# Performance work log

Measured on AMD Instinct MI355X. Metric: run time of the kernel, lower is better.

Reference implementation:

```python
import jax, jax.numpy as jnp
import numpy as np

RADIUS = 0.1
NSAMPLE = 32


def ball_query_cnt(radius, nsample, xyz, new_xyz):
    """xyz: (B,N,3), new_xyz: (B,npoint,3) -> cnt (B,npoint) int32, idx (B,npoint,nsample) int32.
    Matches pointnet2 CUDA semantics: first `nsample` in-radius points in index order;
    unfilled slots replicate the first found index (0 if none found)."""
    N = xyz.shape[1]
    # (B, npoint, N) squared distances
    d2 = jnp.sum((new_xyz[:, :, None, :] - xyz[:, None, :, :]) ** 2, axis=-1)
    mask = d2 < radius * radius
    pos = jnp.arange(N, dtype=jnp.int32)
    # key encodes position so that top_k returns the LOWEST valid positions first
    key = jnp.where(mask, N - pos, -N)
    topk_vals, _ = jax.lax.top_k(key, nsample)          # (B, npoint, nsample)
    valid = topk_vals > 0
    idx = (N - topk_vals).astype(jnp.int32)
    first = jnp.where(valid[..., :1], idx[..., :1], 0)   # fill value per query
    idx = jnp.where(valid, idx, first)
    cnt = jnp.minimum(mask.sum(axis=-1), nsample).astype(jnp.int32)
    return cnt, idx


def group(features, idx):
    """features: (B,C,N), idx: (B,npoint,nsample) -> (B,C,npoint,nsample)."""
    return jax.vmap(lambda f, i: f[:, i])(features, idx)


def setup_inputs() -> dict:
    key = jax.random.key(0)
    k1, k2, k3 = jax.random.split(key, 3)
    B, N, npoint, C = 4, 16384, 2048, 64
    xyz = jax.random.uniform(k1, (B, N, 3), dtype=jnp.float32)
    new_xyz = jax.random.uniform(k2, (B, npoint, 3), dtype=jnp.float32)
    features = jax.random.normal(k3, (B, C, N), dtype=jnp.float32)
    return {"xyz": xyz, "new_xyz": new_xyz, "features": features}


def reference(xyz, new_xyz, features):
    idx_cnt, idx = ball_query_cnt(RADIUS, NSAMPLE, xyz, new_xyz)
    xyz_t = jnp.transpose(xyz, (0, 2, 1))                      # (B,3,N)
    grouped_xyz = group(xyz_t, idx)                            # (B,3,npoint,nsample)
    grouped_xyz = grouped_xyz - jnp.transpose(new_xyz, (0, 2, 1))[..., None]
    grouped_features = group(features, idx)                    # (B,C,npoint,nsample)
    new_features = jnp.concatenate([grouped_xyz, grouped_features], axis=1)
    return idx_cnt, new_features
```

## Files before the change

kernel.cpp:

```cpp
#include <hip/hip_runtime.h>

#define B        4
#define N        16384
#define NPOINT   2048
#define C        64
#define NSAMPLE  32
#define CH       (C + 3)
#define RADIUS2  0.01f
#define NCELL    1000
#define CSTRIDE  1032
#define CCSTRIDE 1024
#define CAP      192

__device__ __forceinline__ int clamp10(int v) {
    return v < 0 ? 0 : (v > 9 ? 9 : v);
}

__global__ __launch_bounds__(256) void transpose_count_kernel(
    const float* __restrict__ xyz,
    const float* __restrict__ f,
    float* __restrict__ ft,
    int* __restrict__ cc)
{
    const int t = threadIdx.x;

    if (blockIdx.x >= 1024) {
        const int g = (blockIdx.x - 1024) * 256 + t;
        const int b = g >> 14;
        const float x = xyz[g * 3 + 0], y = xyz[g * 3 + 1], z = xyz[g * 3 + 2];
        const int cx = clamp10((int)(x * 10.f));
        const int cy = clamp10((int)(y * 10.f));
        const int cz = clamp10((int)(z * 10.f));
        atomicAdd(&cc[(b << 10) + (cx * 10 + cy) * 10 + cz], 1);
        return;
    }

    const int tt = blockIdx.x;
    const int b  = tt >> 8;
    const int n0 = (tt & 255) * 64;

    __shared__ float tile[64][65];
    const int r16 = t >> 4;
    const int x4  = t & 15;
    #pragma unroll
    for (int it = 0; it < 4; ++it) {
        const int cch = it * 16 + r16;
        const float4 v = *(const float4*)(f + ((size_t)b * C + cch) * N + n0 + x4 * 4);
        tile[cch][x4 * 4 + 0] = v.x;
        tile[cch][x4 * 4 + 1] = v.y;
        tile[cch][x4 * 4 + 2] = v.z;
        tile[cch][x4 * 4 + 3] = v.w;
    }
    __syncthreads();
    #pragma unroll
    for (int it = 0; it < 4; ++it) {
        const int nn = it * 16 + r16;
        float4 v;
        v.x = tile[x4 * 4 + 0][nn];
        v.y = tile[x4 * 4 + 1][nn];
        v.z = tile[x4 * 4 + 2][nn];
        v.w = tile[x4 * 4 + 3][nn];
        *(float4*)(ft + ((size_t)b * N + n0 + nn) * C + x4 * 4) = v;
    }
}

__global__ __launch_bounds__(1024) void prefix_kernel(int* __restrict__ cnt,
                                                      int* __restrict__ cs) {
    __shared__ int s[1024];
    const int t = threadIdx.x, b = blockIdx.x;
    const int v = (t < NCELL) ? cnt[(b << 10) + t] : 0;
    s[t] = v;
    __syncthreads();
    for (int off = 1; off < 1024; off <<= 1) {
        const int u = (t >= off) ? s[t - off] : 0;
        __syncthreads();
        s[t] += u;
        __syncthreads();
    }
    const int excl = (t == 0) ? 0 : s[t - 1];
    if (t <= NCELL) cs[b * CSTRIDE + t] = excl;
    if (t < NCELL)  cnt[(b << 10) + t] = excl;
}

__global__ __launch_bounds__(256) void scatter_kernel(const float* __restrict__ xyz,
                                                      int* __restrict__ cursor,
                                                      float4* __restrict__ sp) {
    const int g = blockIdx.x * 256 + threadIdx.x;
    const int b = g >> 14;
    const int n = g & (N - 1);
    const float x = xyz[g * 3 + 0], y = xyz[g * 3 + 1], z = xyz[g * 3 + 2];
    const int cx = clamp10((int)(x * 10.f));
    const int cy = clamp10((int)(y * 10.f));
    const int cz = clamp10((int)(z * 10.f));
    const int cell = (cx * 10 + cy) * 10 + cz;
    const int pos = atomicAdd(&cursor[(b << 10) + cell], 1);
    sp[(b << 14) + pos] = make_float4(x, y, z, __int_as_float(n));
}

__global__ __launch_bounds__(256, 8) void qg_kernel(
    const float*  __restrict__ xyz,
    const float*  __restrict__ new_xyz,
    const float*  __restrict__ ft,
    const int*    __restrict__ cs,
    const float4* __restrict__ sp,
    float* __restrict__ out_cnt,
    float* __restrict__ out_feat)
{
    const int w = threadIdx.x >> 6;
    const int l = threadIdx.x & 63;
    const int q = blockIdx.x * 4 + w;
    const int b = q >> 11;
    const int j = q & (NPOINT - 1);

    __shared__ int cand_s[4][CAP];
    __shared__ int sidx_s[4][NSAMPLE];
    int* cand  = cand_s[w];
    int* s_idx = sidx_s[w];

    const float qx = new_xyz[q * 3 + 0];
    const float qy = new_xyz[q * 3 + 1];
    const float qz = new_xyz[q * 3 + 2];

    const int cx = clamp10((int)(qx * 10.f));
    const int cy = clamp10((int)(qy * 10.f));
    const int cz = clamp10((int)(qz * 10.f));
    const int z0 = cz > 0 ? cz - 1 : 0;
    const int z1 = cz < 9 ? cz + 1 : 9;

    int sv = 0, ev = 0;
    if (l < 9) {
        const int xx = cx - 1 + l / 3;
        const int yy = cy - 1 + l % 3;
        if (xx >= 0 && xx <= 9 && yy >= 0 && yy <= 9) {
            const int cb = (xx * 10 + yy) * 10;
            sv = cs[b * CSTRIDE + cb + z0];
            ev = cs[b * CSTRIDE + cb + z1 + 1];
        }
    }
    const int len = ev - sv;

    int S[9], L[9];
    #pragma unroll
    for (int r = 0; r < 9; ++r) {
        S[r] = __builtin_amdgcn_readlane(sv, r);
        L[r] = __builtin_amdgcn_readlane(len, r);
    }
    int T = 0;
    #pragma unroll
    for (int r = 0; r < 9; ++r) T += L[r];

    const unsigned long long ltmask = (1ull << l) - 1ull;
    int total = 0, ncand = 0;
    for (int base = 0; base < T; base += 64) {
        const int wid = base + l;
        int p = 0, acc = 0;
        bool act = false;
        #pragma unroll
        for (int r = 0; r < 9; ++r) {
            const int off = wid - acc;
            if (off >= 0 && off < L[r]) { p = S[r] + off; act = true; }
            acc += L[r];
        }
        float4 pt = make_float4(1e9f, 1e9f, 1e9f, 0.f);
        if (act) pt = sp[(b << 14) + p];
        const float dx = pt.x - qx, dy = pt.y - qy, dz = pt.z - qz;
        const float d2 = dx * dx + dy * dy + dz * dz;
        const bool in = act && (d2 < RADIUS2);
        const unsigned long long m = __ballot(in);
        if (in) {
            const int slot = ncand + __popcll(m & ltmask);
            if (slot < CAP) cand[slot] = __float_as_int(pt.w);
        }
        const int c = __popcll(m);
        total += c;
        ncand = ncand + c > CAP ? CAP : ncand + c;
    }

    int cntv;
    if (total > CAP) {
        const float* xb = xyz + (size_t)b * N * 3;
        int cnt2 = 0;
        for (int base = 0; base < N; base += 64) {
            const int p = base + l;
            const float dx = xb[p * 3 + 0] - qx;
            const float dy = xb[p * 3 + 1] - qy;
            const float dz = xb[p * 3 + 2] - qz;
            const float d2 = dx * dx + dy * dy + dz * dz;
            const bool in = d2 < RADIUS2;
            const unsigned long long m = __ballot(in);
            if (in) {
                const int slot = cnt2 + __popcll(m & ltmask);
                if (slot < NSAMPLE) s_idx[slot] = p;
            }
            cnt2 += __popcll(m);
            if (cnt2 >= NSAMPLE) break;
        }
        cntv = cnt2 < NSAMPLE ? cnt2 : NSAMPLE;
        __threadfence_block();
    } else {
        __threadfence_block();
        const int K = ncand;
        for (int c = l; c < K; c += 64) {
            const int v = cand[c];
            int rnk = 0;
            for (int i = 0; i < K; ++i) rnk += (cand[i] < v) ? 1 : 0;
            if (rnk < NSAMPLE) s_idx[rnk] = v;
        }
        cntv = total < NSAMPLE ? total : NSAMPLE;
        __threadfence_block();
    }

    if (l < NSAMPLE && l >= cntv) s_idx[l] = (cntv > 0) ? s_idx[0] : 0;
    __threadfence_block();

    if (l == 0) out_cnt[q] = (float)cntv;

    const int k   = l & 31;
    const int i   = s_idx[k];
    const int chh = l >> 5;

    if (l < 32) {
        const float* xp = xyz + ((size_t)b * N + i) * 3;
        float* ob = out_feat + ((size_t)(b * CH) * NPOINT + j) * NSAMPLE + l;
        __builtin_nontemporal_store(xp[0] - qx, ob);
        __builtin_nontemporal_store(xp[1] - qy, ob + NPOINT * NSAMPLE);
        __builtin_nontemporal_store(xp[2] - qz, ob + 2 * NPOINT * NSAMPLE);
    }
    const float* fp = ft + ((size_t)b * N + i) * C + chh;
    float* op = out_feat + ((size_t)(b * CH + 3 + chh) * NPOINT + j) * NSAMPLE + k;
    #pragma unroll 8
    for (int p = 0; p < 32; ++p) {
        __builtin_nontemporal_store(fp[2 * p],
                                    op + (size_t)2 * p * NPOINT * NSAMPLE);
    }
}

__global__ __launch_bounds__(64) void qg_wave_kernel(
    const float* __restrict__ xyz,
    const float* __restrict__ new_xyz,
    const float* __restrict__ feat,
    float* __restrict__ out_cnt,
    float* __restrict__ out_feat)
{
    const int q = blockIdx.x;
    const int b = q >> 11;
    const int j = q & (NPOINT - 1);
    const int l = threadIdx.x;

    __shared__ int s_idx[NSAMPLE];

    const float qx = new_xyz[q * 3 + 0];
    const float qy = new_xyz[q * 3 + 1];
    const float qz = new_xyz[q * 3 + 2];
    const float* xb = xyz + (size_t)b * N * 3;

    int cnt = 0;
    for (int base = 0; base < N; base += 64) {
        const int p = base + l;
        const float dx = xb[p * 3 + 0] - qx;
        const float dy = xb[p * 3 + 1] - qy;
        const float dz = xb[p * 3 + 2] - qz;
        const float d2 = dx * dx + dy * dy + dz * dz;
        const bool in = d2 < RADIUS2;
        const unsigned long long m = __ballot(in);
        if (in) {
            const int slot = cnt + __popcll(m & ((1ull << l) - 1ull));
            if (slot < NSAMPLE) s_idx[slot] = p;
        }
        cnt += __popcll(m);
        if (cnt >= NSAMPLE) break;
    }
    if (cnt > NSAMPLE) cnt = NSAMPLE;

    if (l == 0) out_cnt[q] = (float)cnt;
    __syncthreads();
    if (l < NSAMPLE && l >= cnt) s_idx[l] = (cnt > 0) ? s_idx[0] : 0;
    __syncthreads();

    const int k   = l & 31;
    const int i   = s_idx[k];
    const int chh = l >> 5;
    if (l < 32) {
        const float* xp = xyz + ((size_t)b * N + i) * 3;
        float* ob = out_feat + ((size_t)(b * CH) * NPOINT + j) * NSAMPLE + l;
        ob[0]                   = xp[0] - qx;
        ob[NPOINT * NSAMPLE]     = xp[1] - qy;
        ob[2 * NPOINT * NSAMPLE] = xp[2] - qz;
    }
    const float* fp = feat + ((size_t)b * C + chh) * N + i;
    float* op = out_feat + ((size_t)(b * CH + 3 + chh) * NPOINT + j) * NSAMPLE + k;
    #pragma unroll 8
    for (int p = 0; p < 32; ++p) {
        op[(size_t)2 * p * NPOINT * NSAMPLE] = fp[(size_t)2 * p * N];
    }
}

extern "C" void kernel_launch(void* const* d_in, const int* in_sizes, int n_in,
                              void* d_out, int out_size, void* d_ws, size_t ws_size,
                              hipStream_t stream) {
    const float* xyz      = (const float*)d_in[0];
    const float* new_xyz  = (const float*)d_in[1];
    const float* features = (const float*)d_in[2];

    float* out_cnt  = (float*)d_out;
    float* out_feat = out_cnt + (size_t)B * NPOINT;

    char* ws = (char*)d_ws;
    const size_t ftB = (size_t)B * N * C * sizeof(float);
    const size_t spB = (size_t)B * N * sizeof(float4);
    const size_t csB = (size_t)B * CSTRIDE * sizeof(int);
    const size_t ccB = (size_t)B * CCSTRIDE * sizeof(int);
    const size_t need = ftB + spB + csB + ccB;

    if (ws_size >= need) {
        float*  ft = (float*)ws;
        float4* sp = (float4*)(ws + ftB);
        int*    cs = (int*)(ws + ftB + spB);
        int*    cc = (int*)(ws + ftB + spB + csB);
        hipMemsetAsync(cc, 0, ccB, stream);
        transpose_count_kernel<<<1280, 256, 0, stream>>>(xyz, features, ft, cc);
        prefix_kernel<<<B, 1024, 0, stream>>>(cc, cs);
        scatter_kernel<<<B * N / 256, 256, 0, stream>>>(xyz, cc, sp);
        qg_kernel<<<B * NPOINT / 4, 256, 0, stream>>>(xyz, new_xyz, ft, cs, sp,
                                                      out_cnt, out_feat);
    } else {
        qg_wave_kernel<<<B * NPOINT, 64, 0, stream>>>(xyz, new_xyz, features,
                                                      out_cnt, out_feat);
    }
}
```

Before: 137.7 us.

## Fuse prefix scan into prep kernel via last-block pattern; vectorize gather stores

Merges the transpose/count kernel and the per-batch prefix-scan kernel into one launch. A last-block-done atomic counter (stored in the unused cc[1023] slot) elects one block to run the scan over all four batches. The gather epilogue now has each lane produce a float4 of four consecutive samples for one channel and write it with a single 16-byte nontemporal store, where before each lane wrote scalars. This saves one kernel launch and widens the output writes, at the cost of a serialized single-block scan and a device-wide fence in every block.

Result: slower. 247.7 us (+79.9%).

```diff
diff --git a/kernel.cpp b/kernel.cpp
--- a/kernel.cpp
+++ b/kernel.cpp
@@ -11,18 +11,25 @@
 #define CSTRIDE  1032
 #define CCSTRIDE 1024
 #define CAP      192
+#define K1GRID   1280
+
+typedef float vfloat4 __attribute__((ext_vector_type(4)));
 
 __device__ __forceinline__ int clamp10(int v) {
     return v < 0 ? 0 : (v > 9 ? 9 : v);
 }
 
-__global__ __launch_bounds__(256) void transpose_count_kernel(
+__global__ __launch_bounds__(256) void prep_kernel(
     const float* __restrict__ xyz,
     const float* __restrict__ f,
     float* __restrict__ ft,
-    int* __restrict__ cc)
+    int* __restrict__ cc,
+    int* __restrict__ cs)
 {
     const int t = threadIdx.x;
+    __shared__ float tile[64][65];
+    __shared__ int   wsum[256];
+    __shared__ int   islast;
 
     if (blockIdx.x >= 1024) {
         const int g = (blockIdx.x - 1024) * 256 + t;
@@ -32,54 +39,74 @@
         const int cy = clamp10((int)(y * 10.f));
         const int cz = clamp10((int)(z * 10.f));
         atomicAdd(&cc[(b << 10) + (cx * 10 + cy) * 10 + cz], 1);
-        return;
-    }
-
-    const int tt = blockIdx.x;
-    const int b  = tt >> 8;
-    const int n0 = (tt & 255) * 64;
-
-    __shared__ float tile[64][65];
-    const int r16 = t >> 4;
-    const int x4  = t & 15;
-    #pragma unroll
-    for (int it = 0; it < 4; ++it) {
-        const int cch = it * 16 + r16;
-        const float4 v = *(const float4*)(f + ((size_t)b * C + cch) * N + n0 + x4 * 4);
-        tile[cch][x4 * 4 + 0] = v.x;
-        tile[cch][x4 * 4 + 1] = v.y;
-        tile[cch][x4 * 4 + 2] = v.z;
-        tile[cch][x4 * 4 + 3] = v.w;
-    }
+    } else {
+        const int tt = blockIdx.x;
+        const int b  = tt >> 8;
+        const int n0 = (tt & 255) * 64;
+        const int r16 = t >> 4;
+        const int x4  = t & 15;
+        #pragma unroll
+        for (int it = 0; it < 4; ++it) {
+            const int cch = it * 16 + r16;
+            const float4 v = *(const float4*)(f + ((size_t)b * C + cch) * N + n0 + x4 * 4);
+            tile[cch][x4 * 4 + 0] = v.x;
+            tile[cch][x4 * 4 + 1] = v.y;
+            tile[cch][x4 * 4 + 2] = v.z;
+            tile[cch][x4 * 4 + 3] = v.w;
+        }
+        __syncthreads();
+        #pragma unroll
+        for (int it = 0; it < 4; ++it) {
+            const int nn = it * 16 + r16;
+            float4 v;
+            v.x = tile[x4 * 4 + 0][nn];
+            v.y = tile[x4 * 4 + 1][nn];
+            v.z = tile[x4 * 4 + 2][nn];
+            v.w = tile[x4 * 4 + 3][nn];
+            *(float4*)(ft + ((size_t)b * N + n0 + nn) * C + x4 * 4) = v;
+        }
+    }
+
+    __threadfence();
     __syncthreads();
-    #pragma unroll
-    for (int it = 0; it < 4; ++it) {
-        const int nn = it * 16 + r16;
-        float4 v;
-        v.x = tile[x4 * 4 + 0][nn];
-        v.y = tile[x4 * 4 + 1][nn];
-        v.z = tile[x4 * 4 + 2][nn];
-        v.w = tile[x4 * 4 + 3][nn];
-        *(float4*)(ft + ((size_t)b * N + n0 + nn) * C + x4 * 4) = v;
-    }
-}
-
-__global__ __launch_bounds__(1024) void prefix_kernel(int* __restrict__ cnt,
-                                                      int* __restrict__ cs) {
-    __shared__ int s[1024];
-    const int t = threadIdx.x, b = blockIdx.x;
-    const int v = (t < NCELL) ? cnt[(b << 10) + t] : 0;
-    s[t] = v;
+    if (t == 0) {
+        const int done = atomicAdd(&cc[1023], 1);
+        islast = (done == K1GRID - 1) ? 1 : 0;
+    }
     __syncthreads();
-    for (int off = 1; off < 1024; off <<= 1) {
-        const int u = (t >= off) ? s[t - off] : 0;
+    if (!islast) return;
+
+    for (int bb = 0; bb < B; ++bb) {
+        int h[4];
+        #pragma unroll
+        for (int m = 0; m < 4; ++m) {
+            const int cell = t * 4 + m;
+            h[m] = (cell < NCELL)
+                 ? __hip_atomic_load(&cc[(bb << 10) + cell],
+                                     __ATOMIC_RELAXED, __HIP_MEMORY_SCOPE_AGENT)
+                 : 0;
+        }
+        wsum[t] = h[0] + h[1] + h[2] + h[3];
         __syncthreads();
-        s[t] += u;
+        for (int off = 1; off < 256; off <<= 1) {
+            const int u = (t >= off) ? wsum[t - off] : 0;
+            __syncthreads();
+            wsum[t] += u;
+            __syncthreads();
+        }
+        const int base = (t == 0) ? 0 : wsum[t - 1];
+        const int c0 = base, c1 = c0 + h[0], c2 = c1 + h[1], c3 = c2 + h[2];
+        int* csb = cs + bb * CSTRIDE;
+        csb[t * 4 + 0] = c0;
+        csb[t * 4 + 1] = c1;
+        csb[t * 4 + 2] = c2;
+        csb[t * 4 + 3] = c3;
+        cc[(bb << 10) + t * 4 + 0] = c0;
+        cc[(bb << 10) + t * 4 + 1] = c1;
+        cc[(bb << 10) + t * 4 + 2] = c2;
+        cc[(bb << 10) + t * 4 + 3] = c3;
         __syncthreads();
     }
-    const int excl = (t == 0) ? 0 : s[t - 1];
-    if (t <= NCELL) cs[b * CSTRIDE + t] = excl;
-    if (t < NCELL)  cnt[(b << 10) + t] = excl;
 }
 
 __global__ __launch_bounds__(256) void scatter_kernel(const float* __restrict__ xyz,
@@ -215,23 +242,30 @@
 
     if (l == 0) out_cnt[q] = (float)cntv;
 
-    const int k   = l & 31;
-    const int i   = s_idx[k];
-    const int chh = l >> 5;
-
-    if (l < 32) {
-        const float* xp = xyz + ((size_t)b * N + i) * 3;
-        float* ob = out_feat + ((size_t)(b * CH) * NPOINT + j) * NSAMPLE + l;
-        __builtin_nontemporal_store(xp[0] - qx, ob);
-        __builtin_nontemporal_store(xp[1] - qy, ob + NPOINT * NSAMPLE);
-        __builtin_nontemporal_store(xp[2] - qz, ob + 2 * NPOINT * NSAMPLE);
-    }
-    const float* fp = ft + ((size_t)b * N + i) * C + chh;
-    float* op = out_feat + ((size_t)(b * CH + 3 + chh) * NPOINT + j) * NSAMPLE + k;
-    #pragma unroll 8
-    for (int p = 0; p < 32; ++p) {
-        __builtin_nontemporal_store(fp[2 * p],
-                                    op + (size_t)2 * p * NPOINT * NSAMPLE);
+    for (int e4 = l; e4 < CH * 8; e4 += 64) {
+        const int ch = e4 >> 3;
+        const int k4 = (e4 & 7) * 4;
+        const int i0 = s_idx[k4 + 0];
+        const int i1 = s_idx[k4 + 1];
+        const int i2 = s_idx[k4 + 2];
+        const int i3 = s_idx[k4 + 3];
+        vfloat4 v;
+        if (ch < 3) {
+            const float qc = (ch == 0) ? qx : ((ch == 1) ? qy : qz);
+            v.x = xyz[((size_t)b * N + i0) * 3 + ch] - qc;
+            v.y = xyz[((size_t)b * N + i1) * 3 + ch] - qc;
+            v.z = xyz[((size_t)b * N + i2) * 3 + ch] - qc;
+            v.w = xyz[((size_t)b * N + i3) * 3 + ch] - qc;
+        } else {
+            const int c = ch - 3;
+            v.x = ft[((size_t)b * N + i0) * C + c];
+            v.y = ft[((size_t)b * N + i1) * C + c];
+            v.z = ft[((size_t)b * N + i2) * C + c];
+            v.w = ft[((size_t)b * N + i3) * C + c];
+        }
+        vfloat4* op = (vfloat4*)(out_feat +
+                      ((size_t)(b * CH + ch) * NPOINT + j) * NSAMPLE) + (e4 & 7);
+        __builtin_nontemporal_store(v, op);
     }
 }
 
@@ -277,21 +311,30 @@
     if (l < NSAMPLE && l >= cnt) s_idx[l] = (cnt > 0) ? s_idx[0] : 0;
     __syncthreads();
 
-    const int k   = l & 31;
-    const int i   = s_idx[k];
-    const int chh = l >> 5;
-    if (l < 32) {
-        const float* xp = xyz + ((size_t)b * N + i) * 3;
-        float* ob = out_feat + ((size_t)(b * CH) * NPOINT + j) * NSAMPLE + l;
-        ob[0]                   = xp[0] - qx;
-        ob[NPOINT * NSAMPLE]     = xp[1] - qy;
-        ob[2 * NPOINT * NSAMPLE] = xp[2] - qz;
-    }
-    const float* fp = feat + ((size_t)b * C + chh) * N + i;
-    float* op = out_feat + ((size_t)(b * CH + 3 + chh) * NPOINT + j) * NSAMPLE + k;
-    #pragma unroll 8
-    for (int p = 0; p < 32; ++p) {
-        op[(size_t)2 * p * NPOINT * NSAMPLE] = fp[(size_t)2 * p * N];
+    for (int e4 = l; e4 < CH * 8; e4 += 64) {
+        const int ch = e4 >> 3;
+        const int k4 = (e4 & 7) * 4;
+        const int i0 = s_idx[k4 + 0];
+        const int i1 = s_idx[k4 + 1];
+        const int i2 = s_idx[k4 + 2];
+        const int i3 = s_idx[k4 + 3];
+        float4 v;
+        if (ch < 3) {
+            const float qc = (ch == 0) ? qx : ((ch == 1) ? qy : qz);
+            v.x = xyz[((size_t)b * N + i0) * 3 + ch] - qc;
+            v.y = xyz[((size_t)b * N + i1) * 3 + ch] - qc;
+            v.z = xyz[((size_t)b * N + i2) * 3 + ch] - qc;
+            v.w = xyz[((size_t)b * N + i3) * 3 + ch] - qc;
+        } else {
+            const int c = ch - 3;
+            v.x = feat[((size_t)b * C + c) * N + i0];
+            v.y = feat[((size_t)b * C + c) * N + i1];
+            v.z = feat[((size_t)b * C + c) * N + i2];
+            v.w = feat[((size_t)b * C + c) * N + i3];
+        }
+        float4* op = (float4*)(out_feat +
+                     ((size_t)(b * CH + ch) * NPOINT + j) * NSAMPLE) + (e4 & 7);
+        *op = v;
     }
 }
 
@@ -318,8 +361,7 @@
         int*    cs = (int*)(ws + ftB + spB);
         int*    cc = (int*)(ws + ftB + spB + csB);
         hipMemsetAsync(cc, 0, ccB, stream);
-        transpose_count_kernel<<<1280, 256, 0, stream>>>(xyz, features, ft, cc);
-        prefix_kernel<<<B, 1024, 0, stream>>>(cc, cs);
+        prep_kernel<<<K1GRID, 256, 0, stream>>>(xyz, features, ft, cc, cs);
         scatter_kernel<<<B * N / 256, 256, 0, stream>>>(xyz, cc, sp);
         qg_kernel<<<B * NPOINT / 4, 256, 0, stream>>>(xyz, new_xyz, ft, cs, sp,
                                                       out_cnt, out_feat);
```
